# Kernel optimization log

Measured on AMD Instinct MI355X. Metric: run time of the kernel, lower is better.

Reference implementation:

```python
import jax, jax.numpy as jnp
import numpy as np

NUM_HEAD = 16


def setup_inputs() -> dict:
    key = jax.random.key(0)
    ks = jax.random.split(key, 7)
    B, S, E = 2, 2048, 1024
    scale = 0.02
    return {
        "x": jax.random.normal(ks[0], (B, S, E), dtype=jnp.float32),
        "Wq": jax.random.normal(ks[1], (E, E), dtype=jnp.float32) * scale,
        "bq": jax.random.normal(ks[2], (E,), dtype=jnp.float32) * scale,
        "Wk": jax.random.normal(ks[3], (E, E), dtype=jnp.float32) * scale,
        "bk": jax.random.normal(ks[4], (E,), dtype=jnp.float32) * scale,
        "Wv": jax.random.normal(ks[5], (E, E), dtype=jnp.float32) * scale,
        "bv": jax.random.normal(ks[6], (E,), dtype=jnp.float32) * scale,
    }


def reference(x, Wq, bq, Wk, bk, Wv, bv):
    B, S, E = x.shape
    H = NUM_HEAD
    Dh = E // H
    # torch Linear: y = x @ W.T + b
    q = (x @ Wq.T + bq).reshape(B, S, H, Dh).transpose(0, 2, 1, 3)  # [B,H,S,Dh]
    k = (x @ Wk.T + bk).reshape(B, S, H, Dh).transpose(0, 2, 1, 3)
    v = (x @ Wv.T + bv).reshape(B, S, H, Dh).transpose(0, 2, 1, 3)
    attn = jnp.einsum("bhqd,bhkd->bhqk", q, k) / jnp.sqrt(jnp.float32(Dh))
    score = jax.nn.softmax(attn, axis=-1)
    out = jnp.einsum("bhqk,bhkd->bhqd", score, v)  # [B,H,S,Dh]
    return out.transpose(0, 2, 1, 3).reshape(B, S, E)
```

## Files before the change

kernel.cpp:

```cpp
#include <hip/hip_runtime.h>
#include <hip/hip_bf16.h>
#include <stdint.h>

#define S_LEN 2048
#define E_DIM 1024
#define NHEAD 16
#define DHEAD 64
#define BATCH 2

typedef short bf16x8 __attribute__((ext_vector_type(8)));
typedef float f32x4 __attribute__((ext_vector_type(4)));
typedef float f32x16 __attribute__((ext_vector_type(16)));

__device__ __forceinline__ ushort f2bf(float f) {
    uint32_t u = __builtin_bit_cast(uint32_t, f);
    u += 0x7fffu + ((u >> 16) & 1u);
    return (ushort)(u >> 16);
}
__device__ __forceinline__ uint32_t cvtpk(float lo, float hi) {
    uint32_t r;
    asm("v_cvt_pk_bf16_f32 %0, %1, %2" : "=v"(r) : "v"(lo), "v"(hi));
    return r;
}
__device__ __forceinline__ f32x16 zero16() {
    f32x16 v;
    #pragma unroll
    for (int i = 0; i < 16; ++i) v[i] = 0.f;
    return v;
}
__device__ __forceinline__ void gload16(const void* g, void* l) {
    __builtin_amdgcn_global_load_lds(
        (const __attribute__((address_space(1))) uint32_t*)g,
        (__attribute__((address_space(3))) uint32_t*)l, 16, 0, 0);
}

__global__ __launch_bounds__(256) void convert_kernel(
    const float* __restrict__ x, const float* __restrict__ wq,
    const float* __restrict__ wk, const float* __restrict__ wv,
    ushort* __restrict__ xb, ushort* __restrict__ wqb,
    ushort* __restrict__ wkb, ushort* __restrict__ wvb)
{
    const int a = blockIdx.y;
    const float* src = (a == 0) ? x : (a == 1) ? wq : (a == 2) ? wk : wv;
    ushort* dst      = (a == 0) ? xb : (a == 1) ? wqb : (a == 2) ? wkb : wvb;
    const int n4 = (a == 0) ? (BATCH * S_LEN * E_DIM / 4) : (E_DIM * E_DIM / 4);
    const int idx = blockIdx.x * 256 + threadIdx.x;
    if (idx < n4) {
        float4 v = reinterpret_cast<const float4*>(src)[idx];
        ushort4 o;
        o.x = f2bf(v.x); o.y = f2bf(v.y); o.z = f2bf(v.z); o.w = f2bf(v.w);
        reinterpret_cast<ushort4*>(dst)[idx] = o;
    }
}

__global__ __launch_bounds__(256) void qkv_mfma_kernel(
    const ushort* __restrict__ xb, const ushort* __restrict__ wqb,
    const ushort* __restrict__ wkb, const ushort* __restrict__ wvb,
    const float* __restrict__ bq, const float* __restrict__ bk,
    const float* __restrict__ bv,
    ushort* __restrict__ qb, ushort* __restrict__ kb, ushort* __restrict__ vtb)
{
    const int z = blockIdx.z;
    const ushort* Ag; const ushort* Bg; const float* bias;
    int m0, n0;
    if (z == 2) { Ag = wvb; Bg = xb;                 bias = bv;
                  m0 = blockIdx.y * 128; n0 = blockIdx.x * 128; }
    else        { Ag = xb;  Bg = (z == 0) ? wqb : wkb; bias = (z == 0) ? bq : bk;
                  m0 = blockIdx.x * 128; n0 = blockIdx.y * 128; }

    __shared__ ushort As[128 * 32];
    __shared__ ushort Bs[128 * 32];

    const int tid  = threadIdx.x;
    const int lane = tid & 63;
    const int wid  = tid >> 6;
    const int wr   = wid >> 1, wc = wid & 1;

    f32x4 acc[4][4];
    #pragma unroll
    for (int i = 0; i < 4; ++i)
        #pragma unroll
        for (int j = 0; j < 4; ++j) acc[i][j] = (f32x4){0.f, 0.f, 0.f, 0.f};

    const int grow = lane >> 2;
    const int gcol = (lane & 3) * 8;
    const int lr   = lane & 15;
    const int lc   = (lane >> 4) * 8;

    for (int k0 = 0; k0 < E_DIM; k0 += 32) {
        #pragma unroll
        for (int j = 0; j < 2; ++j) {
            const int rbase = wid * 32 + j * 16;
            gload16(&Ag[(size_t)(m0 + rbase + grow) * E_DIM + k0 + gcol],
                    &As[rbase * 32]);
            gload16(&Bg[(size_t)(n0 + rbase + grow) * E_DIM + k0 + gcol],
                    &Bs[rbase * 32]);
        }
        __syncthreads();

        bf16x8 af[4], bf[4];
        #pragma unroll
        for (int mi = 0; mi < 4; ++mi)
            af[mi] = *reinterpret_cast<const bf16x8*>(
                &As[(wr * 64 + mi * 16 + lr) * 32 + lc]);
        #pragma unroll
        for (int ni = 0; ni < 4; ++ni)
            bf[ni] = *reinterpret_cast<const bf16x8*>(
                &Bs[(wc * 64 + ni * 16 + lr) * 32 + lc]);
        #pragma unroll
        for (int mi = 0; mi < 4; ++mi)
            #pragma unroll
            for (int ni = 0; ni < 4; ++ni)
                acc[mi][ni] = __builtin_amdgcn_mfma_f32_16x16x32_bf16(
                    af[mi], bf[ni], acc[mi][ni], 0, 0, 0);
        __syncthreads();
    }

    const int rq = lane >> 4;
    #pragma unroll
    for (int mi = 0; mi < 4; ++mi) {
        #pragma unroll
        for (int ni = 0; ni < 4; ++ni) {
            #pragma unroll
            for (int r = 0; r < 4; ++r) {
                const int i = m0 + wr * 64 + mi * 16 + rq * 4 + r;
                const int j = n0 + wc * 64 + ni * 16 + lr;
                float val = acc[mi][ni][r];
                if (z == 2) {
                    val += bias[i];
                    const int h = i >> 6, d = i & 63;
                    const int b = j >> 11, s = j & (S_LEN - 1);
                    vtb[(((size_t)(b * NHEAD + h)) * DHEAD + d) * S_LEN + s] = f2bf(val);
                } else {
                    val += bias[j];
                    const int h = j >> 6, d = j & 63;
                    const int b = i >> 11, s = i & (S_LEN - 1);
                    ushort* o = (z == 0) ? qb : kb;
                    o[(((size_t)(b * NHEAD + h)) * S_LEN + s) * DHEAD + d] = f2bf(val);
                }
            }
        }
    }
}

__global__ __launch_bounds__(256) void attn_mfma32_kernel(
    const ushort* __restrict__ qb, const ushort* __restrict__ kb,
    const ushort* __restrict__ vtb, float* __restrict__ out)
{
    const int bid = blockIdx.x;
    const int swzb = (bid & 7) * 64 + (bid >> 3);
    const int bh = swzb >> 4;
    const int q0 = (swzb & 15) * 128;
    const int b = bh >> 4, h = bh & 15;
    const ushort* Q  = qb  + (size_t)bh * S_LEN * DHEAD;
    const ushort* K  = kb  + (size_t)bh * S_LEN * DHEAD;
    const ushort* Vt = vtb + (size_t)bh * DHEAD * S_LEN;

    __shared__ ushort Qs[128 * 64];
    __shared__ ushort KV[2][2 * 64 * 64];

    const int tid  = threadIdx.x;
    const int lane = tid & 63;
    const int wid  = tid >> 6;
    const int hi   = lane >> 5;
    const int l31  = lane & 31;
    const int swzr = (lane & 7) << 3;
    const float CSCALE = 0.125f * 1.4426950408889634f;

    const int stslot = (tid & 7) * 8;
    const int strow  = tid >> 3;

    {
        const int slot = (tid & 7) * 8;
        #pragma unroll
        for (int p = 0; p < 4; ++p) {
            const int row = (tid >> 3) + p * 32;
            bf16x8 v = *reinterpret_cast<const bf16x8*>(
                &Q[(size_t)(q0 + row) * DHEAD + slot]);
            *reinterpret_cast<bf16x8*>(
                &Qs[row * 64 + (slot ^ ((row & 7) << 3))]) = v;
        }
    }

    bf16x8 kreg[2], vreg[2];
    #pragma unroll
    for (int p = 0; p < 2; ++p) {
        const int row = strow + p * 32;
        kreg[p] = *reinterpret_cast<const bf16x8*>(
            &K[(size_t)row * DHEAD + stslot]);
        vreg[p] = *reinterpret_cast<const bf16x8*>(
            &Vt[(size_t)row * S_LEN + stslot]);
    }
    __syncthreads();

    bf16x8 qf[4];
    {
        const int qrow = wid * 32 + l31;
        #pragma unroll
        for (int st = 0; st < 4; ++st)
            qf[st] = *reinterpret_cast<const bf16x8*>(
                &Qs[qrow * 64 + ((st * 16 + hi * 8) ^ swzr)]);
    }

    #pragma unroll
    for (int p = 0; p < 2; ++p) {
        const int row = strow + p * 32;
        const int sw  = row * 64 + (stslot ^ ((row & 7) << 3));
        *reinterpret_cast<bf16x8*>(&KV[0][sw])           = kreg[p];
        *reinterpret_cast<bf16x8*>(&KV[0][64 * 64 + sw]) = vreg[p];
    }
    __syncthreads();

    float m_run = -1e30f, l_run = 0.f;
    f32x16 oacc[2] = {zero16(), zero16()};
    int cur = 0;

    for (int t0 = 0; t0 < S_LEN; t0 += 64) {
        const bool more = (t0 + 64 < S_LEN);
        if (more) {
            const int tn = t0 + 64;
            #pragma unroll
            for (int p = 0; p < 2; ++p) {
                const int row = strow + p * 32;
                kreg[p] = *reinterpret_cast<const bf16x8*>(
                    &K[(size_t)(tn + row) * DHEAD + stslot]);
                vreg[p] = *reinterpret_cast<const bf16x8*>(
                    &Vt[(size_t)row * S_LEN + tn + stslot]);
            }
        }

        const ushort* Ks = &KV[cur][0];
        const ushort* Vs = &KV[cur][64 * 64];

        f32x16 sacc[2] = {zero16(), zero16()};
        #pragma unroll
        for (int t = 0; t < 2; ++t) {
            const int kbase = (t * 32 + l31) * 64;
            #pragma unroll
            for (int st = 0; st < 4; ++st) {
                bf16x8 kf = *reinterpret_cast<const bf16x8*>(
                    &Ks[kbase + ((st * 16 + hi * 8) ^ swzr)]);
                sacc[t] = __builtin_amdgcn_mfma_f32_32x32x16_bf16(
                    kf, qf[st], sacc[t], 0, 0, 0);
            }
        }

        float mx = sacc[0][0];
        #pragma unroll
        for (int r = 1; r < 16; ++r) mx = fmaxf(mx, sacc[0][r]);
        #pragma unroll
        for (int r = 0; r < 16; ++r) mx = fmaxf(mx, sacc[1][r]);
        mx = fmaxf(mx, __shfl_xor(mx, 32));
        const float mt = mx * CSCALE;

        if (__any(mt > m_run + 8.0f)) {
            const float mn = fmaxf(m_run, mt);
            const float al = exp2f(m_run - mn);
            m_run = mn;
            l_run *= al;
            #pragma unroll
            for (int r = 0; r < 16; ++r) { oacc[0][r] *= al; oacc[1][r] *= al; }
        }

        float lsum = 0.f;
        uint32_t w[4][4];
        #pragma unroll
        for (int t = 0; t < 2; ++t) {
            #pragma unroll
            for (int half = 0; half < 2; ++half) {
                float p[8];
                #pragma unroll
                for (int j = 0; j < 8; ++j) {
                    p[j] = exp2f(fmaf(sacc[t][half * 8 + j], CSCALE, -m_run));
                    lsum += p[j];
                }
                const uint32_t a0 = cvtpk(p[0], p[1]);
                const uint32_t a1 = cvtpk(p[2], p[3]);
                const uint32_t b0 = cvtpk(p[4], p[5]);
                const uint32_t b1 = cvtpk(p[6], p[7]);
                const uint32_t xs0 = __shfl_xor(a0, 32);
                const uint32_t ys0 = __shfl_xor(b0, 32);
                const uint32_t xs1 = __shfl_xor(a1, 32);
                const uint32_t ys1 = __shfl_xor(b1, 32);
                const int c = t * 2 + half;
                w[c][0] = hi ? ys0 : a0;
                w[c][2] = hi ? b0  : xs0;
                w[c][1] = hi ? ys1 : a1;
                w[c][3] = hi ? b1  : xs1;
            }
        }
        lsum += __shfl_xor(lsum, 32);
        l_run += lsum;

        #pragma unroll
        for (int c = 0; c < 4; ++c) {
            union { uint32_t u[4]; bf16x8 v; } pf;
            pf.u[0] = w[c][0]; pf.u[1] = w[c][1];
            pf.u[2] = w[c][2]; pf.u[3] = w[c][3];
            #pragma unroll
            for (int dblk = 0; dblk < 2; ++dblk) {
                const int vrow = dblk * 32 + l31;
                bf16x8 vf = *reinterpret_cast<const bf16x8*>(
                    &Vs[vrow * 64 + ((c * 16 + hi * 8) ^ swzr)]);
                oacc[dblk] = __builtin_amdgcn_mfma_f32_32x32x16_bf16(
                    vf, pf.v, oacc[dblk], 0, 0, 0);
            }
        }

        if (more) {
            __syncthreads();
            #pragma unroll
            for (int p = 0; p < 2; ++p) {
                const int row = strow + p * 32;
                const int sw  = row * 64 + (stslot ^ ((row & 7) << 3));
                *reinterpret_cast<bf16x8*>(&KV[cur ^ 1][sw])           = kreg[p];
                *reinterpret_cast<bf16x8*>(&KV[cur ^ 1][64 * 64 + sw]) = vreg[p];
            }
            __syncthreads();
            cur ^= 1;
        }
    }

    const float inv = 1.f / l_run;
    const int qg = q0 + wid * 32 + l31;
    float* obase = &out[((size_t)(b * S_LEN + qg)) * E_DIM + h * DHEAD];
    #pragma unroll
    for (int dblk = 0; dblk < 2; ++dblk) {
        #pragma unroll
        for (int g = 0; g < 4; ++g) {
            float4 f;
            f.x = oacc[dblk][g * 4 + 0] * inv;
            f.y = oacc[dblk][g * 4 + 1] * inv;
            f.z = oacc[dblk][g * 4 + 2] * inv;
            f.w = oacc[dblk][g * 4 + 3] * inv;
            *reinterpret_cast<float4*>(&obase[dblk * 32 + g * 8 + hi * 4]) = f;
        }
    }
}

extern "C" void kernel_launch(void* const* d_in, const int* in_sizes, int n_in,
                              void* d_out, int out_size, void* d_ws, size_t ws_size,
                              hipStream_t stream) {
    const float* x  = (const float*)d_in[0];
    const float* Wq = (const float*)d_in[1];
    const float* bq = (const float*)d_in[2];
    const float* Wk = (const float*)d_in[3];
    const float* bk = (const float*)d_in[4];
    const float* Wv = (const float*)d_in[5];
    const float* bv = (const float*)d_in[6];
    float* out = (float*)d_out;

    const size_t XN = (size_t)BATCH * S_LEN * E_DIM;
    const size_t WN = (size_t)E_DIM * E_DIM;
    ushort* xb  = (ushort*)d_ws;
    ushort* wqb = xb  + XN;
    ushort* wkb = wqb + WN;
    ushort* wvb = wkb + WN;
    ushort* qbb = wvb + WN;
    ushort* kbb = qbb + XN;
    ushort* vtb = kbb + XN;

    convert_kernel<<<dim3(4096, 4), 256, 0, stream>>>(
        x, Wq, Wk, Wv, xb, wqb, wkb, wvb);

    qkv_mfma_kernel<<<dim3(32, 8, 3), 256, 0, stream>>>(
        xb, wqb, wkb, wvb, bq, bk, bv, qbb, kbb, vtb);

    attn_mfma32_kernel<<<dim3(512), 256, 0, stream>>>(qbb, kbb, vtb, out);
}
```

Measured before the change: 195.4 us.

## Deepen QKV GEMM K-tile with swizzled LDS and enlarge attention blocks to 256 queries

The QKV projection GEMM now stages 64-wide K slices per iteration with an XOR-swizzled LDS layout, halving the number of barrier pairs and reducing bank conflicts. The attention kernel switches to 512-thread blocks covering 256 query rows, so each K/V tile loaded into LDS is shared by twice as many waves and each thread loads a single K/V vector. Softmax now uses __expf on base-e scaled scores and computes the row max and sum with tree reductions. The trade-offs are a grid of only 256 attention blocks, which lowers occupancy flexibility and tail balance, and a possible change in exp accuracy.

```diff
diff --git a/kernel.cpp b/kernel.cpp
--- a/kernel.cpp
+++ b/kernel.cpp
@@ -68,8 +68,8 @@
     else        { Ag = xb;  Bg = (z == 0) ? wqb : wkb; bias = (z == 0) ? bq : bk;
                   m0 = blockIdx.x * 128; n0 = blockIdx.y * 128; }
 
-    __shared__ ushort As[128 * 32];
-    __shared__ ushort Bs[128 * 32];
+    __shared__ ushort As[128 * 64];
+    __shared__ ushort Bs[128 * 64];
 
     const int tid  = threadIdx.x;
     const int lane = tid & 63;
@@ -82,37 +82,48 @@
         #pragma unroll
         for (int j = 0; j < 4; ++j) acc[i][j] = (f32x4){0.f, 0.f, 0.f, 0.f};
 
-    const int grow = lane >> 2;
-    const int gcol = (lane & 3) * 8;
-    const int lr   = lane & 15;
-    const int lc   = (lane >> 4) * 8;
-
-    for (int k0 = 0; k0 < E_DIM; k0 += 32) {
-        #pragma unroll
-        for (int j = 0; j < 2; ++j) {
-            const int rbase = wid * 32 + j * 16;
-            gload16(&Ag[(size_t)(m0 + rbase + grow) * E_DIM + k0 + gcol],
-                    &As[rbase * 32]);
-            gload16(&Bg[(size_t)(n0 + rbase + grow) * E_DIM + k0 + gcol],
-                    &Bs[rbase * 32]);
+    const int crow  = lane >> 3;
+    const int cslot = lane & 7;
+    const int lr    = lane & 15;
+    const int lq    = lane >> 4;
+
+    for (int k0 = 0; k0 < E_DIM; k0 += 64) {
+        #pragma unroll
+        for (int j = 0; j < 4; ++j) {
+            const int rbase = wid * 32 + j * 8;
+            const int srow  = rbase + crow;
+            const int sslot = cslot ^ (srow & 7);
+            gload16(&Ag[(size_t)(m0 + srow) * E_DIM + k0 + sslot * 8],
+                    &As[rbase * 64]);
+            gload16(&Bg[(size_t)(n0 + srow) * E_DIM + k0 + sslot * 8],
+                    &Bs[rbase * 64]);
         }
         __syncthreads();
 
-        bf16x8 af[4], bf[4];
-        #pragma unroll
-        for (int mi = 0; mi < 4; ++mi)
-            af[mi] = *reinterpret_cast<const bf16x8*>(
-                &As[(wr * 64 + mi * 16 + lr) * 32 + lc]);
-        #pragma unroll
-        for (int ni = 0; ni < 4; ++ni)
-            bf[ni] = *reinterpret_cast<const bf16x8*>(
-                &Bs[(wc * 64 + ni * 16 + lr) * 32 + lc]);
-        #pragma unroll
-        for (int mi = 0; mi < 4; ++mi)
-            #pragma unroll
-            for (int ni = 0; ni < 4; ++ni)
-                acc[mi][ni] = __builtin_amdgcn_mfma_f32_16x16x32_bf16(
-                    af[mi], bf[ni], acc[mi][ni], 0, 0, 0);
+        #pragma unroll
+        for (int ks = 0; ks < 2; ++ks) {
+            bf16x8 af[4], bf[4];
+            #pragma unroll
+            for (int mi = 0; mi < 4; ++mi) {
+                const int row  = wr * 64 + mi * 16 + lr;
+                const int slot = (ks * 4 + lq) ^ (row & 7);
+                af[mi] = *reinterpret_cast<const bf16x8*>(
+                    &As[row * 64 + slot * 8]);
+            }
+            #pragma unroll
+            for (int ni = 0; ni < 4; ++ni) {
+                const int row  = wc * 64 + ni * 16 + lr;
+                const int slot = (ks * 4 + lq) ^ (row & 7);
+                bf[ni] = *reinterpret_cast<const bf16x8*>(
+                    &Bs[row * 64 + slot * 8]);
+            }
+            #pragma unroll
+            for (int mi = 0; mi < 4; ++mi)
+                #pragma unroll
+                for (int ni = 0; ni < 4; ++ni)
+                    acc[mi][ni] = __builtin_amdgcn_mfma_f32_16x16x32_bf16(
+                        af[mi], bf[ni], acc[mi][ni], 0, 0, 0);
+        }
         __syncthreads();
     }
 
@@ -143,20 +154,20 @@
     }
 }
 
-__global__ __launch_bounds__(256) void attn_mfma32_kernel(
+__global__ __launch_bounds__(512) void attn_mfma32_kernel(
     const ushort* __restrict__ qb, const ushort* __restrict__ kb,
     const ushort* __restrict__ vtb, float* __restrict__ out)
 {
     const int bid = blockIdx.x;
-    const int swzb = (bid & 7) * 64 + (bid >> 3);
-    const int bh = swzb >> 4;
-    const int q0 = (swzb & 15) * 128;
+    const int swzb = (bid & 7) * 32 + (bid >> 3);
+    const int bh = swzb >> 3;
+    const int q0 = (swzb & 7) * 256;
     const int b = bh >> 4, h = bh & 15;
     const ushort* Q  = qb  + (size_t)bh * S_LEN * DHEAD;
     const ushort* K  = kb  + (size_t)bh * S_LEN * DHEAD;
     const ushort* Vt = vtb + (size_t)bh * DHEAD * S_LEN;
 
-    __shared__ ushort Qs[128 * 64];
+    __shared__ ushort Qs[256 * 64];
     __shared__ ushort KV[2][2 * 64 * 64];
 
     const int tid  = threadIdx.x;
@@ -165,32 +176,23 @@
     const int hi   = lane >> 5;
     const int l31  = lane & 31;
     const int swzr = (lane & 7) << 3;
-    const float CSCALE = 0.125f * 1.4426950408889634f;
+    const float SC = 0.125f;
 
     const int stslot = (tid & 7) * 8;
     const int strow  = tid >> 3;
 
-    {
-        const int slot = (tid & 7) * 8;
-        #pragma unroll
-        for (int p = 0; p < 4; ++p) {
-            const int row = (tid >> 3) + p * 32;
-            bf16x8 v = *reinterpret_cast<const bf16x8*>(
-                &Q[(size_t)(q0 + row) * DHEAD + slot]);
-            *reinterpret_cast<bf16x8*>(
-                &Qs[row * 64 + (slot ^ ((row & 7) << 3))]) = v;
-        }
-    }
-
-    bf16x8 kreg[2], vreg[2];
-    #pragma unroll
-    for (int p = 0; p < 2; ++p) {
-        const int row = strow + p * 32;
-        kreg[p] = *reinterpret_cast<const bf16x8*>(
-            &K[(size_t)row * DHEAD + stslot]);
-        vreg[p] = *reinterpret_cast<const bf16x8*>(
-            &Vt[(size_t)row * S_LEN + stslot]);
-    }
+    #pragma unroll
+    for (int p = 0; p < 4; ++p) {
+        const int row = strow + p * 64;
+        bf16x8 v = *reinterpret_cast<const bf16x8*>(
+            &Q[(size_t)(q0 + row) * DHEAD + stslot]);
+        *reinterpret_cast<bf16x8*>(
+            &Qs[row * 64 + (stslot ^ ((row & 7) << 3))]) = v;
+    }
+
+    bf16x8 kreg, vreg;
+    kreg = *reinterpret_cast<const bf16x8*>(&K[(size_t)strow * DHEAD + stslot]);
+    vreg = *reinterpret_cast<const bf16x8*>(&Vt[(size_t)strow * S_LEN + stslot]);
     __syncthreads();
 
     bf16x8 qf[4];
@@ -199,15 +201,13 @@
         #pragma unroll
         for (int st = 0; st < 4; ++st)
             qf[st] = *reinterpret_cast<const bf16x8*>(
-                &Qs[qrow * 64 + ((st * 16 + hi * 8) ^ swzr)]);
-    }
-
-    #pragma unroll
-    for (int p = 0; p < 2; ++p) {
-        const int row = strow + p * 32;
-        const int sw  = row * 64 + (stslot ^ ((row & 7) << 3));
-        *reinterpret_cast<bf16x8*>(&KV[0][sw])           = kreg[p];
-        *reinterpret_cast<bf16x8*>(&KV[0][64 * 64 + sw]) = vreg[p];
+                &Qs[qrow * 64 + ((st * 16 + hi * 8) ^ ((qrow & 7) << 3))]);
+    }
+
+    {
+        const int sw = strow * 64 + (stslot ^ ((strow & 7) << 3));
+        *reinterpret_cast<bf16x8*>(&KV[0][sw])           = kreg;
+        *reinterpret_cast<bf16x8*>(&KV[0][64 * 64 + sw]) = vreg;
     }
     __syncthreads();
 
@@ -219,14 +219,10 @@
         const bool more = (t0 + 64 < S_LEN);
         if (more) {
             const int tn = t0 + 64;
-            #pragma unroll
-            for (int p = 0; p < 2; ++p) {
-                const int row = strow + p * 32;
-                kreg[p] = *reinterpret_cast<const bf16x8*>(
-                    &K[(size_t)(tn + row) * DHEAD + stslot]);
-                vreg[p] = *reinterpret_cast<const bf16x8*>(
-                    &Vt[(size_t)row * S_LEN + tn + stslot]);
-            }
+            kreg = *reinterpret_cast<const bf16x8*>(
+                &K[(size_t)(tn + strow) * DHEAD + stslot]);
+            vreg = *reinterpret_cast<const bf16x8*>(
+                &Vt[(size_t)strow * S_LEN + tn + stslot]);
         }
 
         const ushort* Ks = &KV[cur][0];
@@ -245,24 +241,26 @@
             }
         }
 
-        float mx = sacc[0][0];
-        #pragma unroll
-        for (int r = 1; r < 16; ++r) mx = fmaxf(mx, sacc[0][r]);
-        #pragma unroll
-        for (int r = 0; r < 16; ++r) mx = fmaxf(mx, sacc[1][r]);
+        float m8[8];
+        #pragma unroll
+        for (int i = 0; i < 8; ++i)
+            m8[i] = fmaxf(fmaxf(sacc[0][i], sacc[0][i + 8]),
+                          fmaxf(sacc[1][i], sacc[1][i + 8]));
+        float mx = fmaxf(fmaxf(fmaxf(m8[0], m8[4]), fmaxf(m8[1], m8[5])),
+                         fmaxf(fmaxf(m8[2], m8[6]), fmaxf(m8[3], m8[7])));
         mx = fmaxf(mx, __shfl_xor(mx, 32));
-        const float mt = mx * CSCALE;
+        const float mt = mx * SC;
 
         if (__any(mt > m_run + 8.0f)) {
             const float mn = fmaxf(m_run, mt);
-            const float al = exp2f(m_run - mn);
+            const float al = __expf(m_run - mn);
             m_run = mn;
             l_run *= al;
             #pragma unroll
             for (int r = 0; r < 16; ++r) { oacc[0][r] *= al; oacc[1][r] *= al; }
         }
 
-        float lsum = 0.f;
+        float csum[4];
         uint32_t w[4][4];
         #pragma unroll
         for (int t = 0; t < 2; ++t) {
@@ -270,10 +268,11 @@
             for (int half = 0; half < 2; ++half) {
                 float p[8];
                 #pragma unroll
-                for (int j = 0; j < 8; ++j) {
-                    p[j] = exp2f(fmaf(sacc[t][half * 8 + j], CSCALE, -m_run));
-                    lsum += p[j];
-                }
+                for (int j = 0; j < 8; ++j)
+                    p[j] = __expf(fmaf(sacc[t][half * 8 + j], SC, -m_run));
+                const int c = t * 2 + half;
+                csum[c] = (p[0] + p[1]) + (p[2] + p[3]) +
+                          ((p[4] + p[5]) + (p[6] + p[7]));
                 const uint32_t a0 = cvtpk(p[0], p[1]);
                 const uint32_t a1 = cvtpk(p[2], p[3]);
                 const uint32_t b0 = cvtpk(p[4], p[5]);
@@ -282,13 +281,13 @@
                 const uint32_t ys0 = __shfl_xor(b0, 32);
                 const uint32_t xs1 = __shfl_xor(a1, 32);
                 const uint32_t ys1 = __shfl_xor(b1, 32);
-                const int c = t * 2 + half;
                 w[c][0] = hi ? ys0 : a0;
                 w[c][2] = hi ? b0  : xs0;
                 w[c][1] = hi ? ys1 : a1;
                 w[c][3] = hi ? b1  : xs1;
             }
         }
+        float lsum = (csum[0] + csum[1]) + (csum[2] + csum[3]);
         lsum += __shfl_xor(lsum, 32);
         l_run += lsum;
 
@@ -309,13 +308,9 @@
 
         if (more) {
             __syncthreads();
-            #pragma unroll
-            for (int p = 0; p < 2; ++p) {
-                const int row = strow + p * 32;
-                const int sw  = row * 64 + (stslot ^ ((row & 7) << 3));
-                *reinterpret_cast<bf16x8*>(&KV[cur ^ 1][sw])           = kreg[p];
-                *reinterpret_cast<bf16x8*>(&KV[cur ^ 1][64 * 64 + sw]) = vreg[p];
-            }
+            const int sw = strow * 64 + (stslot ^ ((strow & 7) << 3));
+            *reinterpret_cast<bf16x8*>(&KV[cur ^ 1][sw])           = kreg;
+            *reinterpret_cast<bf16x8*>(&KV[cur ^ 1][64 * 64 + sw]) = vreg;
             __syncthreads();
             cur ^= 1;
         }
@@ -366,5 +361,5 @@
     qkv_mfma_kernel<<<dim3(32, 8, 3), 256, 0, stream>>>(
         xb, wqb, wkb, wvb, bq, bk, bv, qbb, kbb, vtb);
 
-    attn_mfma32_kernel<<<dim3(512), 256, 0, stream>>>(qbb, kbb, vtb, out);
-}
+    attn_mfma32_kernel<<<dim3(256), 512, 0, stream>>>(qbb, kbb, vtb, out);
+}
```

Result: no change. 196.1 us (+0.3%).
